# Kernel optimization log

Hardware: AMD Instinct MI355X
Metric: run time of the kernel (lower is better)

The kernel has to match this reference:

```python
import jax, jax.numpy as jnp
import numpy as np

NEG_BIG = -9e15
LEAKY_SLOPE = 0.01  # nn.LeakyReLU default

N, IN_DIM, HIDDEN_DIM, OUT_DIM = 16384, 512, 256, 128


def setup_inputs() -> dict:
    key = jax.random.key(0)
    ks = jax.random.split(key, 6)
    # He-ish init scaled like torch Linear defaults (uniform +-1/sqrt(fan_in))
    def lin_init(k, fan_in, fan_out):
        kw, kb = jax.random.split(k)
        bound = 1.0 / np.sqrt(fan_in)
        W = jax.random.uniform(kw, (fan_in, fan_out), jnp.float32, -bound, bound)
        b = jax.random.uniform(kb, (fan_out,), jnp.float32, -bound, bound)
        return W, b
    W1, b1 = lin_init(ks[0], IN_DIM, HIDDEN_DIM)
    W2, b2 = lin_init(ks[1], HIDDEN_DIM, OUT_DIM)
    x = jax.random.normal(ks[2], (N, IN_DIM), jnp.float32)
    return {
        "x": x,
        "g": 0,  # unused graph arg in the executed forward path
        "W1": W1, "b1": b1,
        "W2": W2, "b2": b2,
        "alpha": jnp.array([0.1], jnp.float32),
        "beta": jnp.array([0.9], jnp.float32),
    }


def _sim_agg(x):
    # adj: [N, N] dense similarity
    adj = jnp.matmul(x, x.T)
    a = jnp.where(adj > 0, adj, jnp.float32(NEG_BIG))
    sim1 = jax.nn.softmax(a, axis=1)
    return jnp.matmul(sim1, x)


def reference(x, g, W1, b1, W2, b2, alpha, beta):
    # dropout is inactive in eval mode (F.dropout with training=False)
    h = jnp.matmul(x, W1) + b1
    h = jnp.where(h >= 0, h, LEAKY_SLOPE * h)  # LeakyReLU
    h = jnp.matmul(h, W2) + b2                 # [N, out_dim]
    out = alpha * _sim_agg(h) + beta * h
    return jax.nn.log_softmax(out, axis=1)
```

## Files before the change

kernel.cpp:

```cpp
#include <hip/hip_runtime.h>
#include <hip/hip_bf16.h>

typedef __bf16 bf16_t;
typedef __bf16 bf16x8 __attribute__((ext_vector_type(8)));
typedef __bf16 bf16x4 __attribute__((ext_vector_type(4)));
typedef __bf16 bf16x2 __attribute__((ext_vector_type(2)));
typedef float f32x4 __attribute__((ext_vector_type(4)));
typedef float f32x2 __attribute__((ext_vector_type(2)));
typedef unsigned short u16;

#define NROWS 16384
#define KDIM  512
#define HID   256
#define ODIM  128
#define KS    8
#define LOG2E 1.44269504f

__device__ __forceinline__ f32x4 mfma16(bf16x8 a, bf16x8 b, f32x4 c) {
  return __builtin_amdgcn_mfma_f32_16x16x32_bf16(a, b, c, 0, 0, 0);
}

__device__ __forceinline__ void dma16(const void* g, void* l) {
  __builtin_amdgcn_global_load_lds(
      (const __attribute__((address_space(1))) unsigned int*)g,
      (__attribute__((address_space(3))) unsigned int*)l, 16, 0, 0);
}

__global__ __launch_bounds__(256) void prep(const float* __restrict__ x,
                                            const float* __restrict__ W1,
                                            const float* __restrict__ W2,
                                            bf16_t* __restrict__ xb,
                                            bf16_t* __restrict__ W1T,
                                            bf16_t* __restrict__ W2T) {
  int t = blockIdx.x * 256 + threadIdx.x;
  int stride = gridDim.x * 256;
  for (int e = t; e < NROWS * KDIM / 4; e += stride) {
    f32x4 v = *(const f32x4*)(x + (size_t)e * 4);
    bf16x4 pk;
    pk[0] = (bf16_t)v[0]; pk[1] = (bf16_t)v[1];
    pk[2] = (bf16_t)v[2]; pk[3] = (bf16_t)v[3];
    *(bf16x4*)(xb + (size_t)e * 4) = pk;
  }
  for (int e = t; e < HID * KDIM; e += stride) {
    int n = e >> 9, k = e & 511;
    W1T[e] = (bf16_t)W1[k * HID + n];
  }
  for (int e = t; e < ODIM * HID; e += stride) {
    int n = e >> 8, k = e & 255;
    W2T[e] = (bf16_t)W2[k * ODIM + n];
  }
}

__global__ __launch_bounds__(256) void gemm1(const bf16_t* __restrict__ xb,
                                             const bf16_t* __restrict__ W1T,
                                             const float* __restrict__ b1,
                                             bf16_t* __restrict__ h1) {
  __shared__ u16 As[128 * 40];
  __shared__ u16 Bs[64 * 40];
  int tid = threadIdx.x;
  int lane = tid & 63, w = tid >> 6;
  int r = lane & 15, q = lane >> 4;
  int wm = w & 1, wn = w >> 1;
  int mbase = blockIdx.x * 128, nbase = blockIdx.y * 64;

  f32x4 acc[4][2];
#pragma unroll
  for (int ms = 0; ms < 4; ms++)
#pragma unroll
    for (int ns = 0; ns < 2; ns++) acc[ms][ns] = (f32x4){0.f, 0.f, 0.f, 0.f};

  for (int kb = 0; kb < KDIM; kb += 32) {
#pragma unroll
    for (int i = 0; i < 2; i++) {
      int g = tid + 256 * i;
      int rr = g >> 2, c = (g & 3) * 8;
      *(bf16x8*)&As[rr * 40 + c] =
          *(const bf16x8*)(xb + (size_t)(mbase + rr) * KDIM + kb + c);
    }
    {
      int rr = tid >> 2, c = (tid & 3) * 8;
      *(bf16x8*)&Bs[rr * 40 + c] =
          *(const bf16x8*)(W1T + (size_t)(nbase + rr) * KDIM + kb + c);
    }
    __syncthreads();
    bf16x8 af[4], bfr[2];
#pragma unroll
    for (int ms = 0; ms < 4; ms++)
      af[ms] = *(bf16x8*)&As[(wm * 64 + ms * 16 + r) * 40 + q * 8];
#pragma unroll
    for (int ns = 0; ns < 2; ns++)
      bfr[ns] = *(bf16x8*)&Bs[(wn * 32 + ns * 16 + r) * 40 + q * 8];
#pragma unroll
    for (int ms = 0; ms < 4; ms++)
#pragma unroll
      for (int ns = 0; ns < 2; ns++)
        acc[ms][ns] = mfma16(af[ms], bfr[ns], acc[ms][ns]);
    __syncthreads();
  }
#pragma unroll
  for (int ns = 0; ns < 2; ns++) {
    int col = nbase + wn * 32 + ns * 16 + r;
    float bias = b1[col];
#pragma unroll
    for (int ms = 0; ms < 4; ms++) {
      int row0 = mbase + wm * 64 + ms * 16 + q * 4;
#pragma unroll
      for (int reg = 0; reg < 4; reg++) {
        float v = acc[ms][ns][reg] + bias;
        v = v >= 0.f ? v : 0.01f * v;
        h1[(size_t)(row0 + reg) * HID + col] = (bf16_t)v;
      }
    }
  }
}

__global__ __launch_bounds__(256) void gemm2(const bf16_t* __restrict__ h1,
                                             const bf16_t* __restrict__ W2T,
                                             const float* __restrict__ b2,
                                             bf16_t* __restrict__ hb,
                                             bf16_t* __restrict__ hT) {
  __shared__ u16 As[128 * 40];
  __shared__ u16 Bs[64 * 40];
  int tid = threadIdx.x;
  int lane = tid & 63, w = tid >> 6;
  int r = lane & 15, q = lane >> 4;
  int wm = w & 1, wn = w >> 1;
  int mbase = blockIdx.x * 128, nbase = blockIdx.y * 64;

  f32x4 acc[4][2];
#pragma unroll
  for (int ms = 0; ms < 4; ms++)
#pragma unroll
    for (int ns = 0; ns < 2; ns++) acc[ms][ns] = (f32x4){0.f, 0.f, 0.f, 0.f};

  for (int kb = 0; kb < HID; kb += 32) {
#pragma unroll
    for (int i = 0; i < 2; i++) {
      int g = tid + 256 * i;
      int rr = g >> 2, c = (g & 3) * 8;
      *(bf16x8*)&As[rr * 40 + c] =
          *(const bf16x8*)(h1 + (size_t)(mbase + rr) * HID + kb + c);
    }
    {
      int rr = tid >> 2, c = (tid & 3) * 8;
      *(bf16x8*)&Bs[rr * 40 + c] =
          *(const bf16x8*)(W2T + (size_t)(nbase + rr) * HID + kb + c);
    }
    __syncthreads();
    bf16x8 af[4], bfr[2];
#pragma unroll
    for (int ms = 0; ms < 4; ms++)
      af[ms] = *(bf16x8*)&As[(wm * 64 + ms * 16 + r) * 40 + q * 8];
#pragma unroll
    for (int ns = 0; ns < 2; ns++)
      bfr[ns] = *(bf16x8*)&Bs[(wn * 32 + ns * 16 + r) * 40 + q * 8];
#pragma unroll
    for (int ms = 0; ms < 4; ms++)
#pragma unroll
      for (int ns = 0; ns < 2; ns++)
        acc[ms][ns] = mfma16(af[ms], bfr[ns], acc[ms][ns]);
    __syncthreads();
  }
#pragma unroll
  for (int ns = 0; ns < 2; ns++) {
    int col = nbase + wn * 32 + ns * 16 + r;
    float bias = b2[col];
#pragma unroll
    for (int ms = 0; ms < 4; ms++) {
      int row0 = mbase + wm * 64 + ms * 16 + q * 4;
      bf16x4 pk;
#pragma unroll
      for (int reg = 0; reg < 4; reg++) {
        float v = acc[ms][ns][reg] + bias;
        hb[(size_t)(row0 + reg) * ODIM + col] = (bf16_t)v;
        pk[reg] = (bf16_t)v;
      }
      *(bf16x4*)(hT + (size_t)col * NROWS + row0) = pk;
    }
  }
}

__global__ __launch_bounds__(512, 6) void flash(const bf16_t* __restrict__ hb,
                                                const bf16_t* __restrict__ hT,
                                                bf16_t* __restrict__ OpA,
                                                bf16_t* __restrict__ OpB,
                                                float* __restrict__ Ml) {
  __shared__ __align__(16) u16 KA[8 * 512];
  __shared__ __align__(16) u16 KT[2][8 * 512];
  __shared__ __align__(16) u16 Pm[8 * 16 * 40];

  int tid = threadIdx.x;
  int lane = tid & 63, w = tid >> 6;
  int r = lane & 15, q = lane >> 4;
  int ksplit = blockIdx.x & 7;
  int qtile = blockIdx.x >> 3;
  int qbase = qtile * 128 + w * 16;
  int kbase = ksplit * (NROWS / KS);
  const int niter = (NROWS / KS) / 32;

  const char* gbase = nullptr;
  size_t jmul = 0;
  int ginc = 0;
  u16* dbase = nullptr;
  if (w < 2) {
    gbase = (const char*)(hb + (size_t)(kbase + w * 16 + r) * ODIM + q * 8);
    jmul = 32 * 2;
    ginc = 32 * ODIM * 2;
    dbase = KA + w * 4 * 512;
  } else if (w < 4) {
    gbase = (const char*)(hT + (size_t)((w - 2) * 64 + r) * NROWS + kbase + q * 8);
    jmul = (size_t)16 * NROWS * 2;
    ginc = 32 * 2;
    dbase = KT[0] + (w - 2) * 4 * 512;
  }

  bf16x8 qf[4];
  {
    int qrow = qbase + r;
#pragma unroll
    for (int kk = 0; kk < 4; kk++)
      qf[kk] = *(const bf16x8*)(hb + (size_t)qrow * ODIM + kk * 32 + q * 8);
  }

  f32x4 oa[8];
#pragma unroll
  for (int m8 = 0; m8 < 8; m8++) oa[m8] = (f32x4){0.f, 0.f, 0.f, 0.f};
  float m_run = 0.f, l_run = 0.f;
  float nmlog = 0.f;

  if (w < 4) {
#pragma unroll
    for (int j = 0; j < 4; j++) dma16(gbase + j * jmul, dbase + j * 512);
    gbase += ginc;
  }

  for (int it = 0; it < niter; it++) {
    __syncthreads();

    f32x4 s[2];
    s[0] = (f32x4){0.f, 0.f, 0.f, 0.f};
    s[1] = (f32x4){0.f, 0.f, 0.f, 0.f};
#pragma unroll
    for (int mt = 0; mt < 2; mt++)
#pragma unroll
      for (int kk = 0; kk < 4; kk++) {
        bf16x8 af = *(bf16x8*)&KA[(mt * 4 + kk) * 512 + lane * 8];
        s[mt] = mfma16(af, qf[kk], s[mt]);
      }
    __syncthreads();

    if (it + 1 < niter && w < 4) {
      u16* d = dbase;
      if (w >= 2) d += ((it + 1) & 1) * 4096;
#pragma unroll
      for (int j = 0; j < 4; j++) dma16(gbase + j * jmul, d + j * 512);
      gbase += ginc;
    }

    float mx;
    {
      float m = m_run;
#pragma unroll
      for (int mt = 0; mt < 2; mt++)
#pragma unroll
        for (int reg = 0; reg < 4; reg++) m = fmaxf(m, s[mt][reg]);
      m = fmaxf(m, __shfl_xor(m, 16, 64));
      m = fmaxf(m, __shfl_xor(m, 32, 64));
      mx = m;
    }
    if (__any(mx > m_run + 8.f)) {
      float sc = __builtin_amdgcn_exp2f((m_run - mx) * LOG2E);
      m_run = mx;
      nmlog = -mx * LOG2E;
      l_run *= sc;
#pragma unroll
      for (int m8 = 0; m8 < 8; m8++)
#pragma unroll
        for (int reg = 0; reg < 4; reg++) oa[m8][reg] *= sc;
    }
    {
      float rs = 0.f;
      bf16x4 pk[2];
#pragma unroll
      for (int mt = 0; mt < 2; mt++)
#pragma unroll
        for (int reg = 0; reg < 4; reg++) {
          float v = s[mt][reg];
          float p = __builtin_amdgcn_exp2f(fmaf(v, LOG2E, nmlog));
          p = v > 0.f ? p : 0.f;
          rs += p;
          pk[mt][reg] = (bf16_t)p;
        }
      rs += __shfl_xor(rs, 16, 64);
      rs += __shfl_xor(rs, 32, 64);
      l_run += rs;
#pragma unroll
      for (int mt = 0; mt < 2; mt++)
        *(bf16x4*)&Pm[w * 640 + r * 40 + mt * 16 + q * 4] = pk[mt];
    }

    bf16x8 pf = *(bf16x8*)&Pm[w * 640 + r * 40 + q * 8];
    const u16* kt = KT[it & 1];
#pragma unroll
    for (int m8 = 0; m8 < 8; m8++) {
      bf16x8 af = *(bf16x8*)&kt[m8 * 512 + lane * 8];
      oa[m8] = mfma16(af, pf, oa[m8]);
    }
  }

  bf16_t* op = ksplit < 6 ? OpA + (size_t)ksplit * NROWS * ODIM
                          : OpB + (size_t)(ksplit - 6) * NROWS * ODIM;
  {
    int row = qbase + r;
#pragma unroll
    for (int m8 = 0; m8 < 8; m8++) {
      bf16x4 pk;
#pragma unroll
      for (int reg = 0; reg < 4; reg++) pk[reg] = (bf16_t)oa[m8][reg];
      *(bf16x4*)(op + (size_t)row * ODIM + m8 * 16 + q * 4) = pk;
    }
    if (q == 0) {
      Ml[(ksplit * NROWS + row) * 2 + 0] = m_run;
      Ml[(ksplit * NROWS + row) * 2 + 1] = l_run;
    }
  }
}

__global__ __launch_bounds__(256) void merge_ls(const bf16_t* __restrict__ OpA,
                                                const bf16_t* __restrict__ OpB,
                                                const float* __restrict__ Ml,
                                                const bf16_t* __restrict__ hbf,
                                                const float* __restrict__ alpha_p,
                                                const float* __restrict__ beta_p,
                                                float* __restrict__ out) {
  int tid = threadIdx.x, lane = tid & 63, w = tid >> 6;
  float al = alpha_p[0], be = beta_p[0];
  for (int i = 0; i < 2; i++) {
    int row = blockIdx.x * 8 + w * 2 + i;
    float mk[KS], lk[KS], ak[KS];
    float M = 0.f;
#pragma unroll
    for (int ksp = 0; ksp < KS; ksp++) {
      mk[ksp] = Ml[(ksp * NROWS + row) * 2 + 0];
      lk[ksp] = Ml[(ksp * NROWS + row) * 2 + 1];
      M = fmaxf(M, mk[ksp]);
    }
    float lt = 0.f;
#pragma unroll
    for (int ksp = 0; ksp < KS; ksp++) {
      ak[ksp] = __expf(mk[ksp] - M);
      lt += lk[ksp] * ak[ksp];
    }
    float inv = al / lt;
    int d0 = lane * 2;
    float a0 = 0.f, a1 = 0.f;
#pragma unroll
    for (int ksp = 0; ksp < KS; ksp++) {
      const bf16_t* op = ksp < 6 ? OpA + (size_t)ksp * NROWS * ODIM
                                 : OpB + (size_t)(ksp - 6) * NROWS * ODIM;
      bf16x2 v = *(const bf16x2*)(op + (size_t)row * ODIM + d0);
      a0 += ak[ksp] * (float)v[0];
      a1 += ak[ksp] * (float)v[1];
    }
    bf16x2 hv = *(const bf16x2*)(hbf + (size_t)row * ODIM + d0);
    float v0 = inv * a0 + be * (float)hv[0];
    float v1 = inv * a1 + be * (float)hv[1];
    float mxv = fmaxf(v0, v1);
#pragma unroll
    for (int off = 1; off < 64; off <<= 1) mxv = fmaxf(mxv, __shfl_xor(mxv, off, 64));
    float se = __expf(v0 - mxv) + __expf(v1 - mxv);
#pragma unroll
    for (int off = 1; off < 64; off <<= 1) se += __shfl_xor(se, off, 64);
    float lz = mxv + __logf(se);
    f32x2 st = {v0 - lz, v1 - lz};
    *(f32x2*)(out + (size_t)row * ODIM + d0) = st;
  }
}

extern "C" void kernel_launch(void* const* d_in, const int* in_sizes, int n_in,
                              void* d_out, int out_size, void* d_ws,
                              size_t ws_size, hipStream_t stream) {
  const float* x     = (const float*)d_in[0];
  const float* W1    = (const float*)d_in[2];
  const float* b1    = (const float*)d_in[3];
  const float* W2    = (const float*)d_in[4];
  const float* b2    = (const float*)d_in[5];
  const float* alpha = (const float*)d_in[6];
  const float* beta  = (const float*)d_in[7];

  char* ws = (char*)d_ws;
  bf16_t* xb  = (bf16_t*)(ws + 0);
  bf16_t* W1T = (bf16_t*)(ws + 16777216);
  bf16_t* W2T = (bf16_t*)(ws + 17039360);
  bf16_t* h1  = (bf16_t*)(ws + 17104896);
  bf16_t* hbf = (bf16_t*)(ws + 25493504);
  bf16_t* hT  = (bf16_t*)(ws + 29687808);
  float*  Ml  = (float*)(ws + 33882112);
  bf16_t* OpB = (bf16_t*)(ws + 34930688);
  bf16_t* OpA = (bf16_t*)(ws + 0);
  float* outp = (float*)d_out;

  prep<<<1024, 256, 0, stream>>>(x, W1, W2, xb, W1T, W2T);
  gemm1<<<dim3(128, 4), 256, 0, stream>>>(xb, W1T, b1, h1);
  gemm2<<<dim3(128, 2), 256, 0, stream>>>(h1, W2T, b2, hbf, hT);
  flash<<<128 * KS, 512, 0, stream>>>(hbf, hT, OpA, OpB, Ml);
  merge_ls<<<2048, 256, 0, stream>>>(OpA, OpB, Ml, hbf, alpha, beta, outp);
}
```

Measured before the change: 299.0 us.

## Fuse the two MLP GEMMs into one kernel keeping hidden activations in LDS

```diff
diff --git a/kernel.cpp b/kernel.cpp
--- a/kernel.cpp
+++ b/kernel.cpp
@@ -51,127 +51,112 @@
   }
 }
 
-__global__ __launch_bounds__(256) void gemm1(const bf16_t* __restrict__ xb,
-                                             const bf16_t* __restrict__ W1T,
-                                             const float* __restrict__ b1,
-                                             bf16_t* __restrict__ h1) {
-  __shared__ u16 As[128 * 40];
-  __shared__ u16 Bs[64 * 40];
+__global__ __launch_bounds__(256) void gemm12(const bf16_t* __restrict__ xb,
+                                              const bf16_t* __restrict__ W1T,
+                                              const float* __restrict__ b1,
+                                              const bf16_t* __restrict__ W2T,
+                                              const float* __restrict__ b2,
+                                              bf16_t* __restrict__ hb,
+                                              bf16_t* __restrict__ hT) {
+  __shared__ u16 As[32 * 40];
+  __shared__ u16 Bs[256 * 40];
+  __shared__ u16 H1s[32 * 264];
   int tid = threadIdx.x;
   int lane = tid & 63, w = tid >> 6;
   int r = lane & 15, q = lane >> 4;
-  int wm = w & 1, wn = w >> 1;
-  int mbase = blockIdx.x * 128, nbase = blockIdx.y * 64;
-
-  f32x4 acc[4][2];
-#pragma unroll
-  for (int ms = 0; ms < 4; ms++)
-#pragma unroll
-    for (int ns = 0; ns < 2; ns++) acc[ms][ns] = (f32x4){0.f, 0.f, 0.f, 0.f};
+  int mbase = blockIdx.x * 32;
+
+  f32x4 acc1[2][4];
+#pragma unroll
+  for (int ms = 0; ms < 2; ms++)
+#pragma unroll
+    for (int ns = 0; ns < 4; ns++) acc1[ms][ns] = (f32x4){0.f, 0.f, 0.f, 0.f};
 
   for (int kb = 0; kb < KDIM; kb += 32) {
+    if (tid < 128) {
+      int rr = tid >> 2, c = (tid & 3) * 8;
+      *(bf16x8*)&As[rr * 40 + c] =
+          *(const bf16x8*)(xb + (size_t)(mbase + rr) * KDIM + kb + c);
+    }
+#pragma unroll
+    for (int i = 0; i < 4; i++) {
+      int g = tid + 256 * i;
+      int rr = g >> 2, c = (g & 3) * 8;
+      *(bf16x8*)&Bs[rr * 40 + c] =
+          *(const bf16x8*)(W1T + (size_t)rr * KDIM + kb + c);
+    }
+    __syncthreads();
+    bf16x8 af[2], bfr[4];
+#pragma unroll
+    for (int ms = 0; ms < 2; ms++)
+      af[ms] = *(bf16x8*)&As[(ms * 16 + r) * 40 + q * 8];
+#pragma unroll
+    for (int ns = 0; ns < 4; ns++)
+      bfr[ns] = *(bf16x8*)&Bs[(w * 64 + ns * 16 + r) * 40 + q * 8];
+#pragma unroll
+    for (int ms = 0; ms < 2; ms++)
+#pragma unroll
+      for (int ns = 0; ns < 4; ns++)
+        acc1[ms][ns] = mfma16(af[ms], bfr[ns], acc1[ms][ns]);
+    __syncthreads();
+  }
+#pragma unroll
+  for (int ns = 0; ns < 4; ns++) {
+    int col = w * 64 + ns * 16 + r;
+    float bias = b1[col];
+#pragma unroll
+    for (int ms = 0; ms < 2; ms++) {
+      int row0 = ms * 16 + q * 4;
+#pragma unroll
+      for (int reg = 0; reg < 4; reg++) {
+        float v = acc1[ms][ns][reg] + bias;
+        v = v >= 0.f ? v : 0.01f * v;
+        *(bf16_t*)&H1s[(row0 + reg) * 264 + col] = (bf16_t)v;
+      }
+    }
+  }
+  __syncthreads();
+
+  f32x4 acc2[2][2];
+#pragma unroll
+  for (int ms = 0; ms < 2; ms++)
+#pragma unroll
+    for (int ns = 0; ns < 2; ns++) acc2[ms][ns] = (f32x4){0.f, 0.f, 0.f, 0.f};
+
+  for (int kb = 0; kb < HID; kb += 32) {
 #pragma unroll
     for (int i = 0; i < 2; i++) {
       int g = tid + 256 * i;
       int rr = g >> 2, c = (g & 3) * 8;
-      *(bf16x8*)&As[rr * 40 + c] =
-          *(const bf16x8*)(xb + (size_t)(mbase + rr) * KDIM + kb + c);
-    }
-    {
-      int rr = tid >> 2, c = (tid & 3) * 8;
       *(bf16x8*)&Bs[rr * 40 + c] =
-          *(const bf16x8*)(W1T + (size_t)(nbase + rr) * KDIM + kb + c);
-    }
-    __syncthreads();
-    bf16x8 af[4], bfr[2];
-#pragma unroll
-    for (int ms = 0; ms < 4; ms++)
-      af[ms] = *(bf16x8*)&As[(wm * 64 + ms * 16 + r) * 40 + q * 8];
+          *(const bf16x8*)(W2T + (size_t)rr * HID + kb + c);
+    }
+    __syncthreads();
+    bf16x8 af2[2], bfr2[2];
+#pragma unroll
+    for (int ms = 0; ms < 2; ms++)
+      af2[ms] = *(bf16x8*)&H1s[(ms * 16 + r) * 264 + kb + q * 8];
 #pragma unroll
     for (int ns = 0; ns < 2; ns++)
-      bfr[ns] = *(bf16x8*)&Bs[(wn * 32 + ns * 16 + r) * 40 + q * 8];
-#pragma unroll
-    for (int ms = 0; ms < 4; ms++)
+      bfr2[ns] = *(bf16x8*)&Bs[(w * 32 + ns * 16 + r) * 40 + q * 8];
+#pragma unroll
+    for (int ms = 0; ms < 2; ms++)
 #pragma unroll
       for (int ns = 0; ns < 2; ns++)
-        acc[ms][ns] = mfma16(af[ms], bfr[ns], acc[ms][ns]);
+        acc2[ms][ns] = mfma16(af2[ms], bfr2[ns], acc2[ms][ns]);
     __syncthreads();
   }
 #pragma unroll
   for (int ns = 0; ns < 2; ns++) {
-    int col = nbase + wn * 32 + ns * 16 + r;
-    float bias = b1[col];
-#pragma unroll
-    for (int ms = 0; ms < 4; ms++) {
-      int row0 = mbase + wm * 64 + ms * 16 + q * 4;
+    int col = w * 32 + ns * 16 + r;
+    float bias = b2[col];
+#pragma unroll
+    for (int ms = 0; ms < 2; ms++) {
+      int row0 = mbase + ms * 16 + q * 4;
+      bf16x4 pk;
 #pragma unroll
       for (int reg = 0; reg < 4; reg++) {
-        float v = acc[ms][ns][reg] + bias;
-        v = v >= 0.f ? v : 0.01f * v;
-        h1[(size_t)(row0 + reg) * HID + col] = (bf16_t)v;
-      }
-    }
-  }
-}
-
-__global__ __launch_bounds__(256) void gemm2(const bf16_t* __restrict__ h1,
-                                             const bf16_t* __restrict__ W2T,
-                                             const float* __restrict__ b2,
-                                             bf16_t* __restrict__ hb,
-                                             bf16_t* __restrict__ hT) {
-  __shared__ u16 As[128 * 40];
-  __shared__ u16 Bs[64 * 40];
-  int tid = threadIdx.x;
-  int lane = tid & 63, w = tid >> 6;
-  int r = lane & 15, q = lane >> 4;
-  int wm = w & 1, wn = w >> 1;
-  int mbase = blockIdx.x * 128, nbase = blockIdx.y * 64;
-
-  f32x4 acc[4][2];
-#pragma unroll
-  for (int ms = 0; ms < 4; ms++)
-#pragma unroll
-    for (int ns = 0; ns < 2; ns++) acc[ms][ns] = (f32x4){0.f, 0.f, 0.f, 0.f};
-
-  for (int kb = 0; kb < HID; kb += 32) {
-#pragma unroll
-    for (int i = 0; i < 2; i++) {
-      int g = tid + 256 * i;
-      int rr = g >> 2, c = (g & 3) * 8;
-      *(bf16x8*)&As[rr * 40 + c] =
-          *(const bf16x8*)(h1 + (size_t)(mbase + rr) * HID + kb + c);
-    }
-    {
-      int rr = tid >> 2, c = (tid & 3) * 8;
-      *(bf16x8*)&Bs[rr * 40 + c] =
-          *(const bf16x8*)(W2T + (size_t)(nbase + rr) * HID + kb + c);
-    }
-    __syncthreads();
-    bf16x8 af[4], bfr[2];
-#pragma unroll
-    for (int ms = 0; ms < 4; ms++)
-      af[ms] = *(bf16x8*)&As[(wm * 64 + ms * 16 + r) * 40 + q * 8];
-#pragma unroll
-    for (int ns = 0; ns < 2; ns++)
-      bfr[ns] = *(bf16x8*)&Bs[(wn * 32 + ns * 16 + r) * 40 + q * 8];
-#pragma unroll
-    for (int ms = 0; ms < 4; ms++)
-#pragma unroll
-      for (int ns = 0; ns < 2; ns++)
-        acc[ms][ns] = mfma16(af[ms], bfr[ns], acc[ms][ns]);
-    __syncthreads();
-  }
-#pragma unroll
-  for (int ns = 0; ns < 2; ns++) {
-    int col = nbase + wn * 32 + ns * 16 + r;
-    float bias = b2[col];
-#pragma unroll
-    for (int ms = 0; ms < 4; ms++) {
-      int row0 = mbase + wm * 64 + ms * 16 + q * 4;
-      bf16x4 pk;
-#pragma unroll
-      for (int reg = 0; reg < 4; reg++) {
-        float v = acc[ms][ns][reg] + bias;
+        float v = acc2[ms][ns][reg] + bias;
         hb[(size_t)(row0 + reg) * ODIM + col] = (bf16_t)v;
         pk[reg] = (bf16_t)v;
       }
@@ -392,7 +377,6 @@
   bf16_t* xb  = (bf16_t*)(ws + 0);
   bf16_t* W1T = (bf16_t*)(ws + 16777216);
   bf16_t* W2T = (bf16_t*)(ws + 17039360);
-  bf16_t* h1  = (bf16_t*)(ws + 17104896);
   bf16_t* hbf = (bf16_t*)(ws + 25493504);
   bf16_t* hT  = (bf16_t*)(ws + 29687808);
   float*  Ml  = (float*)(ws + 33882112);
@@ -401,8 +385,7 @@
   float* outp = (float*)d_out;
 
   prep<<<1024, 256, 0, stream>>>(x, W1, W2, xb, W1T, W2T);
-  gemm1<<<dim3(128, 4), 256, 0, stream>>>(xb, W1T, b1, h1);
-  gemm2<<<dim3(128, 2), 256, 0, stream>>>(h1, W2T, b2, hbf, hT);
+  gemm12<<<512, 256, 0, stream>>>(xb, W1T, b1, W2T, b2, hbf, hT);
   flash<<<128 * KS, 512, 0, stream>>>(hbf, hT, OpA, OpB, Ml);
   merge_ls<<<2048, 256, 0, stream>>>(OpA, OpB, Ml, hbf, alpha, beta, outp);
 }
```

New measurement: 302.2 us. Within noise of the previous version (+1.1%).
